# Kernel tuning notes

Measured on AMD Instinct MI355X. Metric: run time of the kernel, lower is better.

## Reference

```python
import jax, jax.numpy as jnp
import numpy as np

EPS = 1e-10


def setup_inputs() -> dict:
    key = jax.random.key(0)
    ks = jax.random.split(key, 8)
    N, C, H, W = 32, 512, 14, 14
    D, HID = 2048, 256
    s1 = 1.0 / np.sqrt(C + D)
    s2 = 1.0 / np.sqrt(HID)
    return {
        "local_feature": jax.random.normal(ks[0], (N, C, H, W), jnp.float32),
        "global_feature": jax.random.normal(ks[1], (N, D, 1, 1), jnp.float32),
        "W1": jax.random.normal(ks[2], (C + D, HID), jnp.float32) * s1,
        "b1": jnp.zeros((HID,), jnp.float32),
        "W2": jax.random.normal(ks[3], (HID, HID), jnp.float32) * s2,
        "b2": jnp.zeros((HID,), jnp.float32),
        "W3": jax.random.normal(ks[4], (HID, 1), jnp.float32) * s2,
        "b3": jnp.zeros((1,), jnp.float32),
    }


def reference(local_feature, global_feature, W1, b1, W2, b2, W3, b3):
    # Vectorized form of DMIEstimator.calculate_mi (the per-sample Python loop
    # collapsed into one batched pass with a block-diagonal negative mask).
    N, C, H, W = local_feature.shape
    hw = H * W
    nhw = N * hw
    D = global_feature.shape[1]

    lf = jnp.transpose(local_feature, (0, 2, 3, 1)).reshape(nhw, C)   # [nhw, C]
    gf = global_feature[:, :, 0, 0]                                   # [N, D]

    # combined = cat([global, local], -1); split the first Linear accordingly
    # so the [N*nhw, C+D] concat tensor is never materialized.
    h_loc = lf @ W1[D:]                        # [nhw, HID]
    h_glb = gf @ W1[:D] + b1                   # [N, HID]
    h1 = jax.nn.relu(h_glb[:, None, :] + h_loc[None, :, :])  # [N, nhw, HID]
    h2 = jax.nn.relu(h1 @ W2 + b2)                            # [N, nhw, HID]
    scores = (h2 @ W3)[..., 0] + b3[0]                        # [N, nhw]

    mx = jnp.max(scores, axis=1, keepdims=True)               # [N, 1]
    ex = jnp.exp(scores - mx)

    # negatives for sample i exclude its own hw block [hw*i, hw*(i+1))
    own = (jnp.arange(nhw)[None, :] // hw) == jnp.arange(N)[:, None]  # [N, nhw]
    neg_mean = jnp.where(own, 0.0, ex).sum(axis=1) / (nhw - hw) + EPS  # [N]

    # positive (diagonal) block of scores: scores[i, hw*i : hw*(i+1)]
    pos = scores.reshape(N, N, hw)[jnp.arange(N), jnp.arange(N)]       # [N, hw]

    mi = pos - mx - jnp.log(neg_mean)[:, None]                         # [N, hw]
    return mi.reshape(N, H, W)
```

## Files before the change

kernel.cpp:

```cpp
#include <hip/hip_runtime.h>
#include <math.h>

#define NB   32
#define CC   512
#define DD   2048
#define HWP  196
#define NHW  6272
#define HID  256

typedef _Float16 h8 __attribute__((ext_vector_type(8)));
typedef _Float16 h4 __attribute__((ext_vector_type(4)));
typedef float    f4 __attribute__((ext_vector_type(4)));
union F4H8 { f4 f; h8 h; };

__device__ __forceinline__ int fragIdx(int j, int k) {
    return ((j >> 6) << 14) + (((k >> 5) * 4 + ((j & 63) >> 4)) << 9)
         + (((((k >> 3) & 3) << 4) + (j & 15)) << 3) + (k & 7);
}

__global__ __launch_bounds__(256) void prep_kernel(const float* __restrict__ lf,
                                                   const float* __restrict__ gf,
                                                   const float* __restrict__ W1,
                                                   const float* __restrict__ W2,
                                                   float* __restrict__ hpart,
                                                   _Float16* __restrict__ W2F,
                                                   _Float16* __restrict__ W1F,
                                                   _Float16* __restrict__ lf16T) {
    int bid = blockIdx.x, tid = threadIdx.x;
    if (bid < 512) {
        int i = bid >> 4, ky = bid & 15, k = tid;
        const float* g = gf + (size_t)i * DD + ky * 128;
        const float* w = W1 + (size_t)(ky * 128) * HID + k;
        float a0 = 0.f, a1 = 0.f, a2 = 0.f, a3 = 0.f;
        #pragma unroll 8
        for (int r = 0; r < 128; r += 4) {
            a0 = fmaf(g[r + 0], w[(size_t)(r + 0) * HID], a0);
            a1 = fmaf(g[r + 1], w[(size_t)(r + 1) * HID], a1);
            a2 = fmaf(g[r + 2], w[(size_t)(r + 2) * HID], a2);
            a3 = fmaf(g[r + 3], w[(size_t)(r + 3) * HID], a3);
        }
        hpart[((size_t)i * 16 + ky) * HID + k] = (a0 + a1) + (a2 + a3);
    } else if (bid < 608) {
        int tg = (bid - 512) * 256 + tid;
        if (tg < 8192) {
            int t = tg, F = t >> 6, l = t & 63;
            int k2t = F >> 3, ks = F & 7;
            int kb = ks * 32 + (l >> 4) * 8;
            int n  = k2t * 16 + (l & 15);
            _Float16* o = W2F + (size_t)t * 8;
            #pragma unroll
            for (int j = 0; j < 8; j++) o[j] = (_Float16)W2[(size_t)(kb + j) * HID + n];
        } else {
            int t = tg - 8192, F = t >> 6, l = t & 63;
            int k2t = F >> 4, ks = F & 15;
            int kb = ks * 32 + (l >> 4) * 8;
            int n  = k2t * 16 + (l & 15);
            const float* W1c = W1 + (size_t)DD * HID;
            _Float16* o = W1F + (size_t)t * 8;
            #pragma unroll
            for (int j = 0; j < 8; j++) o[j] = (_Float16)W1c[(size_t)(kb + j) * HID + n];
        }
    } else {
        __shared__ _Float16 sT[64][HWP + 4];
        int b = bid - 608;
        int n = b >> 3, c0 = (b & 7) * 64;
        for (int task = tid; task < 64 * 49; task += 256) {
            int c = task / 49, f = task - c * 49;
            f4 v = *(const f4*)&lf[((size_t)n * CC + c0 + c) * HWP + f * 4];
            h4 o = { (_Float16)v.x, (_Float16)v.y, (_Float16)v.z, (_Float16)v.w };
            *(h4*)&sT[c][f * 4] = o;
        }
        __syncthreads();
        for (int task = tid; task < 8 * HWP; task += 256) {
            int ch = task / HWP, p = task - ch * HWP;
            h8 o;
            #pragma unroll
            for (int cc = 0; cc < 8; cc++) o[cc] = sT[ch * 8 + cc][p];
            *(h8*)&lf16T[((size_t)(n * HWP + p)) * CC + c0 + ch * 8] = o;
        }
    }
}

__global__ __launch_bounds__(256, 2) void hlocF_kernel(const _Float16* __restrict__ lf16T,
                                                       const _Float16* __restrict__ W1F,
                                                       const float* __restrict__ hpart,
                                                       const float* __restrict__ b1,
                                                       _Float16* __restrict__ g16,
                                                       _Float16* __restrict__ hF) {
    if (blockIdx.x == 196) {
        int kh = blockIdx.y;
        for (int x = threadIdx.x; x < 16 * HID; x += 256) {
            int i = kh * 16 + (x >> 8), k = x & 255;
            float s = b1[k];
            #pragma unroll
            for (int ky = 0; ky < 16; ky++) s += hpart[((size_t)i * 16 + ky) * HID + k];
            g16[(size_t)i * HID + k] = (_Float16)s;
        }
        return;
    }
    __shared__ _Float16 sLf[32][CC + 16];
    int tid = threadIdx.x;
    int w = tid >> 6, l = tid & 63, quad = l >> 4, ln = l & 15;
    int j0 = blockIdx.x * 32;
    int khalf = blockIdx.y;

    #pragma unroll
    for (int s = 0; s < 8; s++) {
        int y = s * 256 + tid;
        int row = y >> 6, col = (y & 63) * 8;
        h8 v = *(const h8*)&lf16T[(size_t)(j0 + row) * CC + col];
        *(h8*)&sLf[row][col] = v;
    }

    F4H8 Af[32];
    {
        const f4* src = (const f4*)W1F + l;
        #pragma unroll
        for (int mt = 0; mt < 2; mt++)
            #pragma unroll
            for (int ks = 0; ks < 16; ks++)
                Af[mt * 16 + ks].f = src[(size_t)((khalf * 8 + w * 2 + mt) * 16 + ks) * 64];
    }
    __syncthreads();

    f4 acc[4] = {};
    #pragma unroll
    for (int ks = 0; ks < 16; ks++) {
        h8 bF[2];
        #pragma unroll
        for (int nt = 0; nt < 2; nt++)
            bF[nt] = *(const h8*)&sLf[nt * 16 + ln][ks * 32 + quad * 8];
        #pragma unroll
        for (int mt = 0; mt < 2; mt++)
            #pragma unroll
            for (int nt = 0; nt < 2; nt++)
                acc[mt * 2 + nt] = __builtin_amdgcn_mfma_f32_16x16x32_f16(Af[mt * 16 + ks].h, bF[nt], acc[mt * 2 + nt], 0, 0, 0);
    }

    #pragma unroll
    for (int mt = 0; mt < 2; mt++)
        #pragma unroll
        for (int nt = 0; nt < 2; nt++)
            #pragma unroll
            for (int r = 0; r < 4; r++) {
                int j  = j0 + nt * 16 + ln;
                int k2 = khalf * 128 + w * 32 + mt * 16 + quad * 4 + r;
                hF[fragIdx(j, k2)] = (_Float16)acc[mt * 2 + nt][r];
            }
}

__global__ __launch_bounds__(512, 4) void score_kernel(const _Float16* __restrict__ hF,
                                                       const _Float16* __restrict__ g16,
                                                       const _Float16* __restrict__ W2F,
                                                       const float* __restrict__ b2,
                                                       const float* __restrict__ W3,
                                                       const float* __restrict__ b3,
                                                       float* __restrict__ scores) {
    __shared__ _Float16 sA[128 * HID];
    __shared__ float sRed[128][12];
    int tid = threadIdx.x, w = tid >> 6, l = tid & 63, quad = l >> 4, ln = l & 15;
    int bid = blockIdx.x;
    int i = bid & 31, jt = bid >> 5;

    F4H8 Af[16];
    {
        const f4* src = (const f4*)W2F + l;
        #pragma unroll
        for (int mt = 0; mt < 2; mt++)
            #pragma unroll
            for (int ks = 0; ks < 8; ks++)
                Af[mt * 8 + ks].f = src[(size_t)((w * 2 + mt) * 8 + ks) * 64];
    }
    const _Float16* gbase = g16 + (size_t)i * HID;
    float bias3 = b3[0];

    {
        const _Float16* hbase = hF + (size_t)(jt * 2) * 16384;
        h8 z = {};
        #pragma unroll
        for (int s = 0; s < 8; s++) {
            int y  = s * 512 + tid;
            int y2 = y & 2047;
            h8 hv = *(const h8*)&hbase[y * 8];
            h8 gq = *(const h8*)&gbase[(y2 >> 8) * 32 + ((y2 >> 4) & 3) * 8];
            *(h8*)&sA[y * 8] = __builtin_elementwise_max(hv + gq, z);
        }
    }
    __syncthreads();

    #pragma unroll 1
    for (int pass = 0; pass < 4; pass++) {
        f4 acc[4];
        #pragma unroll
        for (int mt = 0; mt < 2; mt++) {
            f4 bv = *(const f4*)&b2[w * 32 + mt * 16 + quad * 4];
            #pragma unroll
            for (int nt = 0; nt < 2; nt++) acc[mt * 2 + nt] = bv;
        }
        #pragma unroll
        for (int ks = 0; ks < 8; ks++) {
            #pragma unroll
            for (int nt = 0; nt < 2; nt++) {
                int ntg = pass * 2 + nt;
                int base = (ntg >= 4) ? 16384 + (ks * 4 + (ntg - 4)) * 512
                                      : (ks * 4 + ntg) * 512;
                h8 hz = *(const h8*)&sA[base + l * 8];
                #pragma unroll
                for (int mt = 0; mt < 2; mt++)
                    acc[mt * 2 + nt] = __builtin_amdgcn_mfma_f32_16x16x32_f16(Af[mt * 8 + ks].h, hz, acc[mt * 2 + nt], 0, 0, 0);
            }
        }
        #pragma unroll
        for (int nt = 0; nt < 2; nt++) {
            float s = 0.f;
            #pragma unroll
            for (int mt = 0; mt < 2; mt++) {
                f4 w3v = *(const f4*)&W3[w * 32 + mt * 16 + quad * 4];
                s += fmaxf(acc[mt * 2 + nt][0], 0.f) * w3v.x
                   + fmaxf(acc[mt * 2 + nt][1], 0.f) * w3v.y
                   + fmaxf(acc[mt * 2 + nt][2], 0.f) * w3v.z
                   + fmaxf(acc[mt * 2 + nt][3], 0.f) * w3v.w;
            }
            s += __shfl_xor(s, 16, 64);
            s += __shfl_xor(s, 32, 64);
            if (quad == 0) sRed[(pass * 2 + nt) * 16 + ln][w] = s;
        }
    }
    __syncthreads();
    if (tid < 128) {
        f4 a = *(const f4*)&sRed[tid][0];
        f4 b = *(const f4*)&sRed[tid][4];
        scores[(size_t)i * NHW + jt * 128 + tid] =
            a.x + a.y + a.z + a.w + b.x + b.y + b.z + b.w + bias3;
    }
}

__global__ __launch_bounds__(1024) void reduce_kernel(const float* __restrict__ scores,
                                                      float* __restrict__ out) {
    int i = blockIdx.x, tid = threadIdx.x;
    const float* row = scores + (size_t)i * NHW;
    const f4* row4 = (const f4*)row;
    __shared__ float sW[16], sW2[16], sval[2];
    float mx = -1e30f;
    for (int q = tid; q < 1568; q += 1024) {
        f4 v = row4[q];
        mx = fmaxf(mx, fmaxf(fmaxf(v.x, v.y), fmaxf(v.z, v.w)));
    }
    #pragma unroll
    for (int off = 32; off > 0; off >>= 1) mx = fmaxf(mx, __shfl_down(mx, off, 64));
    if ((tid & 63) == 0) sW[tid >> 6] = mx;
    __syncthreads();
    if (tid == 0) {
        float m = sW[0];
        for (int c = 1; c < 16; c++) m = fmaxf(m, sW[c]);
        sval[0] = m;
    }
    __syncthreads();
    mx = sval[0];
    int q0 = i * 49, q1 = q0 + 49;
    float tot = 0.f, ownv = 0.f;
    for (int q = tid; q < 1568; q += 1024) {
        f4 v = row4[q];
        float e = expf(v.x - mx) + expf(v.y - mx) + expf(v.z - mx) + expf(v.w - mx);
        tot += e;
        if (q >= q0 && q < q1) ownv += e;
    }
    #pragma unroll
    for (int off = 32; off > 0; off >>= 1) {
        tot  += __shfl_down(tot, off, 64);
        ownv += __shfl_down(ownv, off, 64);
    }
    if ((tid & 63) == 0) { sW[tid >> 6] = tot; sW2[tid >> 6] = ownv; }
    __syncthreads();
    if (tid == 0) {
        float t = 0.f, o = 0.f;
        for (int c = 0; c < 16; c++) { t += sW[c]; o += sW2[c]; }
        float neg_mean = (t - o) / (float)(NHW - HWP) + 1e-10f;
        sval[1] = mx + logf(neg_mean);
    }
    __syncthreads();
    float sub = sval[1];
    if (tid < HWP) out[(size_t)i * HWP + tid] = row[i * HWP + tid] - sub;
}

extern "C" void kernel_launch(void* const* d_in, const int* in_sizes, int n_in,
                              void* d_out, int out_size, void* d_ws, size_t ws_size,
                              hipStream_t stream) {
    const float* lf = (const float*)d_in[0];
    const float* gf = (const float*)d_in[1];
    const float* W1 = (const float*)d_in[2];
    const float* b1 = (const float*)d_in[3];
    const float* W2 = (const float*)d_in[4];
    const float* b2 = (const float*)d_in[5];
    const float* W3 = (const float*)d_in[6];
    const float* b3 = (const float*)d_in[7];
    float* out = (float*)d_out;

    char* ws = (char*)d_ws;
    _Float16* hF     = (_Float16*)ws;
    _Float16* g16    = (_Float16*)(ws + 3211264);
    _Float16* W2F    = (_Float16*)(ws + 3227648);
    _Float16* W1F    = (_Float16*)(ws + 3358720);
    _Float16* lf16T  = (_Float16*)(ws + 3620864);
    float*    scores = (float*)   (ws + 10043392);
    float*    hpart  = (float*)   (ws + 10846208);

    hipLaunchKernelGGL(prep_kernel, dim3(864), dim3(256), 0, stream,
                       lf, gf, W1, W2, hpart, W2F, W1F, lf16T);
    hipLaunchKernelGGL(hlocF_kernel, dim3(197, 2), dim3(256), 0, stream,
                       lf16T, W1F, hpart, b1, g16, hF);
    hipLaunchKernelGGL(score_kernel, dim3(1568), dim3(512), 0, stream,
                       hF, g16, W2F, b2, W3, b3, scores);
    hipLaunchKernelGGL(reduce_kernel, dim3(NB), dim3(1024), 0, stream, scores, out);
}
```

Measured before the change: 120.9 us.

## Reuse staged h_loc tile across two samples and fuse relu-add into MFMA loop

The score kernel now uses 256-thread blocks with 4 waves, each owning 64 hidden rows and holding 32 W2 fragments in registers. Each block stages its raw h_loc tile in LDS once and processes two global samples, applying the global add and ReLU on the fly right before each MFMA. This replaces the per-sample restaging and halves the per-block W2 register loads relative to the work done. hlocF output stores are also vectorized to 4-half writes. In exchange it raises register pressure (32 fragments plus 8 accumulators), redoes the add/relu per pass, and adds extra block syncs.

```diff
diff --git a/kernel.cpp b/kernel.cpp
--- a/kernel.cpp
+++ b/kernel.cpp
@@ -140,16 +140,16 @@
     #pragma unroll
     for (int mt = 0; mt < 2; mt++)
         #pragma unroll
-        for (int nt = 0; nt < 2; nt++)
-            #pragma unroll
-            for (int r = 0; r < 4; r++) {
-                int j  = j0 + nt * 16 + ln;
-                int k2 = khalf * 128 + w * 32 + mt * 16 + quad * 4 + r;
-                hF[fragIdx(j, k2)] = (_Float16)acc[mt * 2 + nt][r];
-            }
-}
-
-__global__ __launch_bounds__(512, 4) void score_kernel(const _Float16* __restrict__ hF,
+        for (int nt = 0; nt < 2; nt++) {
+            int j  = j0 + nt * 16 + ln;
+            int k2 = khalf * 128 + w * 32 + mt * 16 + quad * 4;
+            h4 o = { (_Float16)acc[mt * 2 + nt][0], (_Float16)acc[mt * 2 + nt][1],
+                     (_Float16)acc[mt * 2 + nt][2], (_Float16)acc[mt * 2 + nt][3] };
+            *(h4*)&hF[fragIdx(j, k2)] = o;
+        }
+}
+
+__global__ __launch_bounds__(256, 2) void score_kernel(const _Float16* __restrict__ hF,
                                                        const _Float16* __restrict__ g16,
                                                        const _Float16* __restrict__ W2F,
                                                        const float* __restrict__ b2,
@@ -157,81 +157,85 @@
                                                        const float* __restrict__ b3,
                                                        float* __restrict__ scores) {
     __shared__ _Float16 sA[128 * HID];
-    __shared__ float sRed[128][12];
+    __shared__ float sRed[4][132];
     int tid = threadIdx.x, w = tid >> 6, l = tid & 63, quad = l >> 4, ln = l & 15;
-    int bid = blockIdx.x;
-    int i = bid & 31, jt = bid >> 5;
-
-    F4H8 Af[16];
+    int i0 = blockIdx.x * 2, jt = blockIdx.y;
+
+    F4H8 Af[32];
     {
         const f4* src = (const f4*)W2F + l;
         #pragma unroll
-        for (int mt = 0; mt < 2; mt++)
+        for (int mt = 0; mt < 4; mt++)
             #pragma unroll
             for (int ks = 0; ks < 8; ks++)
-                Af[mt * 8 + ks].f = src[(size_t)((w * 2 + mt) * 8 + ks) * 64];
-    }
-    const _Float16* gbase = g16 + (size_t)i * HID;
+                Af[mt * 8 + ks].f = src[(size_t)((w * 4 + mt) * 8 + ks) * 64];
+    }
+    {
+        const _Float16* hbase = hF + (size_t)jt * 32768;
+        #pragma unroll
+        for (int s = 0; s < 16; s++) {
+            int y = s * 256 + tid;
+            *(h8*)&sA[y * 8] = *(const h8*)&hbase[y * 8];
+        }
+    }
     float bias3 = b3[0];
-
-    {
-        const _Float16* hbase = hF + (size_t)(jt * 2) * 16384;
-        h8 z = {};
-        #pragma unroll
-        for (int s = 0; s < 8; s++) {
-            int y  = s * 512 + tid;
-            int y2 = y & 2047;
-            h8 hv = *(const h8*)&hbase[y * 8];
-            h8 gq = *(const h8*)&gbase[(y2 >> 8) * 32 + ((y2 >> 4) & 3) * 8];
-            *(h8*)&sA[y * 8] = __builtin_elementwise_max(hv + gq, z);
-        }
-    }
+    h8 z = {};
     __syncthreads();
 
     #pragma unroll 1
-    for (int pass = 0; pass < 4; pass++) {
-        f4 acc[4];
-        #pragma unroll
-        for (int mt = 0; mt < 2; mt++) {
-            f4 bv = *(const f4*)&b2[w * 32 + mt * 16 + quad * 4];
-            #pragma unroll
-            for (int nt = 0; nt < 2; nt++) acc[mt * 2 + nt] = bv;
-        }
-        #pragma unroll
-        for (int ks = 0; ks < 8; ks++) {
+    for (int ii = 0; ii < 2; ii++) {
+        int i = i0 + ii;
+        const _Float16* gbase = g16 + (size_t)i * HID;
+        h8 gF[8];
+        #pragma unroll
+        for (int ks = 0; ks < 8; ks++)
+            gF[ks] = *(const h8*)&gbase[ks * 32 + quad * 8];
+
+        #pragma unroll 1
+        for (int pass = 0; pass < 4; pass++) {
+            f4 acc[8];
+            #pragma unroll
+            for (int mt = 0; mt < 4; mt++) {
+                f4 bv = *(const f4*)&b2[w * 64 + mt * 16 + quad * 4];
+                acc[mt * 2 + 0] = bv;
+                acc[mt * 2 + 1] = bv;
+            }
+            #pragma unroll
+            for (int ks = 0; ks < 8; ks++) {
+                #pragma unroll
+                for (int nt = 0; nt < 2; nt++) {
+                    int ntg = pass * 2 + nt;
+                    int base = (ntg >= 4) ? 16384 + (ks * 4 + (ntg - 4)) * 512
+                                          : (ks * 4 + ntg) * 512;
+                    h8 hz = *(const h8*)&sA[base + l * 8];
+                    h8 h1 = __builtin_elementwise_max(hz + gF[ks], z);
+                    #pragma unroll
+                    for (int mt = 0; mt < 4; mt++)
+                        acc[mt * 2 + nt] = __builtin_amdgcn_mfma_f32_16x16x32_f16(Af[mt * 8 + ks].h, h1, acc[mt * 2 + nt], 0, 0, 0);
+                }
+            }
             #pragma unroll
             for (int nt = 0; nt < 2; nt++) {
-                int ntg = pass * 2 + nt;
-                int base = (ntg >= 4) ? 16384 + (ks * 4 + (ntg - 4)) * 512
-                                      : (ks * 4 + ntg) * 512;
-                h8 hz = *(const h8*)&sA[base + l * 8];
+                float s = 0.f;
                 #pragma unroll
-                for (int mt = 0; mt < 2; mt++)
-                    acc[mt * 2 + nt] = __builtin_amdgcn_mfma_f32_16x16x32_f16(Af[mt * 8 + ks].h, hz, acc[mt * 2 + nt], 0, 0, 0);
+                for (int mt = 0; mt < 4; mt++) {
+                    f4 w3v = *(const f4*)&W3[w * 64 + mt * 16 + quad * 4];
+                    s += fmaxf(acc[mt * 2 + nt][0], 0.f) * w3v.x
+                       + fmaxf(acc[mt * 2 + nt][1], 0.f) * w3v.y
+                       + fmaxf(acc[mt * 2 + nt][2], 0.f) * w3v.z
+                       + fmaxf(acc[mt * 2 + nt][3], 0.f) * w3v.w;
+                }
+                s += __shfl_xor(s, 16, 64);
+                s += __shfl_xor(s, 32, 64);
+                if (quad == 0) sRed[w][(pass * 2 + nt) * 16 + ln] = s;
             }
         }
-        #pragma unroll
-        for (int nt = 0; nt < 2; nt++) {
-            float s = 0.f;
-            #pragma unroll
-            for (int mt = 0; mt < 2; mt++) {
-                f4 w3v = *(const f4*)&W3[w * 32 + mt * 16 + quad * 4];
-                s += fmaxf(acc[mt * 2 + nt][0], 0.f) * w3v.x
-                   + fmaxf(acc[mt * 2 + nt][1], 0.f) * w3v.y
-                   + fmaxf(acc[mt * 2 + nt][2], 0.f) * w3v.z
-                   + fmaxf(acc[mt * 2 + nt][3], 0.f) * w3v.w;
-            }
-            s += __shfl_xor(s, 16, 64);
-            s += __shfl_xor(s, 32, 64);
-            if (quad == 0) sRed[(pass * 2 + nt) * 16 + ln][w] = s;
-        }
-    }
-    __syncthreads();
-    if (tid < 128) {
-        f4 a = *(const f4*)&sRed[tid][0];
-        f4 b = *(const f4*)&sRed[tid][4];
-        scores[(size_t)i * NHW + jt * 128 + tid] =
-            a.x + a.y + a.z + a.w + b.x + b.y + b.z + b.w + bias3;
+        __syncthreads();
+        if (tid < 128) {
+            scores[(size_t)i * NHW + jt * 128 + tid] =
+                sRed[0][tid] + sRed[1][tid] + sRed[2][tid] + sRed[3][tid] + bias3;
+        }
+        __syncthreads();
     }
 }
 
@@ -309,7 +313,7 @@
                        lf, gf, W1, W2, hpart, W2F, W1F, lf16T);
     hipLaunchKernelGGL(hlocF_kernel, dim3(197, 2), dim3(256), 0, stream,
                        lf16T, W1F, hpart, b1, g16, hF);
-    hipLaunchKernelGGL(score_kernel, dim3(1568), dim3(512), 0, stream,
+    hipLaunchKernelGGL(score_kernel, dim3(16, 49), dim3(256), 0, stream,
                        hF, g16, W2F, b2, W3, b3, scores);
     hipLaunchKernelGGL(reduce_kernel, dim3(NB), dim3(1024), 0, stream, scores, out);
 }
```

Result: slower. 127.1 us (+5.1%).

## Retile score kernel to 64 columns × 2 samples, vectorize hF stores, online softmax reduce

Applied to the files above, without the earlier changes.

The score kernel now covers a 64-column local tile for two global samples per block. The W2 fragments loaded into registers are reused across both samples, and shared memory per block is halved, so more blocks can be resident at once. The hlocF epilogue writes four halfs in one vector store instead of four scalar stores. The reduce kernel merges its max and exp-sum passes into a single online-softmax pass. The costs are extra exps in the reduction and two more block-wide barriers per sample in the score kernel.

```diff
diff --git a/kernel.cpp b/kernel.cpp
--- a/kernel.cpp
+++ b/kernel.cpp
@@ -140,13 +140,13 @@
     #pragma unroll
     for (int mt = 0; mt < 2; mt++)
         #pragma unroll
-        for (int nt = 0; nt < 2; nt++)
-            #pragma unroll
-            for (int r = 0; r < 4; r++) {
-                int j  = j0 + nt * 16 + ln;
-                int k2 = khalf * 128 + w * 32 + mt * 16 + quad * 4 + r;
-                hF[fragIdx(j, k2)] = (_Float16)acc[mt * 2 + nt][r];
-            }
+        for (int nt = 0; nt < 2; nt++) {
+            int j  = j0 + nt * 16 + ln;
+            int k2 = khalf * 128 + w * 32 + mt * 16 + quad * 4;
+            h4 o = { (_Float16)acc[mt * 2 + nt][0], (_Float16)acc[mt * 2 + nt][1],
+                     (_Float16)acc[mt * 2 + nt][2], (_Float16)acc[mt * 2 + nt][3] };
+            *(h4*)&hF[fragIdx(j, k2)] = o;
+        }
 }
 
 __global__ __launch_bounds__(512, 4) void score_kernel(const _Float16* __restrict__ hF,
@@ -156,11 +156,10 @@
                                                        const float* __restrict__ W3,
                                                        const float* __restrict__ b3,
                                                        float* __restrict__ scores) {
-    __shared__ _Float16 sA[128 * HID];
-    __shared__ float sRed[128][12];
+    __shared__ _Float16 sA[64 * HID];
+    __shared__ float sRed[8][68];
     int tid = threadIdx.x, w = tid >> 6, l = tid & 63, quad = l >> 4, ln = l & 15;
-    int bid = blockIdx.x;
-    int i = bid & 31, jt = bid >> 5;
+    int i0 = blockIdx.x * 2, jt = blockIdx.y;
 
     F4H8 Af[16];
     {
@@ -171,67 +170,68 @@
             for (int ks = 0; ks < 8; ks++)
                 Af[mt * 8 + ks].f = src[(size_t)((w * 2 + mt) * 8 + ks) * 64];
     }
-    const _Float16* gbase = g16 + (size_t)i * HID;
+    const _Float16* hbase = hF + (size_t)jt * 16384;
     float bias3 = b3[0];
-
-    {
-        const _Float16* hbase = hF + (size_t)(jt * 2) * 16384;
-        h8 z = {};
-        #pragma unroll
-        for (int s = 0; s < 8; s++) {
-            int y  = s * 512 + tid;
-            int y2 = y & 2047;
+    h8 z = {};
+
+    #pragma unroll 1
+    for (int ii = 0; ii < 2; ii++) {
+        int i = i0 + ii;
+        const _Float16* gbase = g16 + (size_t)i * HID;
+
+        #pragma unroll
+        for (int s = 0; s < 4; s++) {
+            int y = s * 512 + tid;
             h8 hv = *(const h8*)&hbase[y * 8];
-            h8 gq = *(const h8*)&gbase[(y2 >> 8) * 32 + ((y2 >> 4) & 3) * 8];
+            h8 gq = *(const h8*)&gbase[(y >> 8) * 32 + ((y >> 4) & 3) * 8];
             *(h8*)&sA[y * 8] = __builtin_elementwise_max(hv + gq, z);
         }
-    }
-    __syncthreads();
-
-    #pragma unroll 1
-    for (int pass = 0; pass < 4; pass++) {
-        f4 acc[4];
-        #pragma unroll
-        for (int mt = 0; mt < 2; mt++) {
-            f4 bv = *(const f4*)&b2[w * 32 + mt * 16 + quad * 4];
-            #pragma unroll
-            for (int nt = 0; nt < 2; nt++) acc[mt * 2 + nt] = bv;
-        }
-        #pragma unroll
-        for (int ks = 0; ks < 8; ks++) {
+        __syncthreads();
+
+        #pragma unroll 1
+        for (int pass = 0; pass < 2; pass++) {
+            f4 acc[4];
+            #pragma unroll
+            for (int mt = 0; mt < 2; mt++) {
+                f4 bv = *(const f4*)&b2[w * 32 + mt * 16 + quad * 4];
+                acc[mt * 2 + 0] = bv;
+                acc[mt * 2 + 1] = bv;
+            }
+            #pragma unroll
+            for (int ks = 0; ks < 8; ks++) {
+                #pragma unroll
+                for (int nt = 0; nt < 2; nt++) {
+                    int ntg = pass * 2 + nt;
+                    h8 hz = *(const h8*)&sA[(ks * 4 + ntg) * 512 + l * 8];
+                    #pragma unroll
+                    for (int mt = 0; mt < 2; mt++)
+                        acc[mt * 2 + nt] = __builtin_amdgcn_mfma_f32_16x16x32_f16(Af[mt * 8 + ks].h, hz, acc[mt * 2 + nt], 0, 0, 0);
+                }
+            }
             #pragma unroll
             for (int nt = 0; nt < 2; nt++) {
-                int ntg = pass * 2 + nt;
-                int base = (ntg >= 4) ? 16384 + (ks * 4 + (ntg - 4)) * 512
-                                      : (ks * 4 + ntg) * 512;
-                h8 hz = *(const h8*)&sA[base + l * 8];
+                float s = 0.f;
                 #pragma unroll
-                for (int mt = 0; mt < 2; mt++)
-                    acc[mt * 2 + nt] = __builtin_amdgcn_mfma_f32_16x16x32_f16(Af[mt * 8 + ks].h, hz, acc[mt * 2 + nt], 0, 0, 0);
+                for (int mt = 0; mt < 2; mt++) {
+                    f4 w3v = *(const f4*)&W3[w * 32 + mt * 16 + quad * 4];
+                    s += fmaxf(acc[mt * 2 + nt][0], 0.f) * w3v.x
+                       + fmaxf(acc[mt * 2 + nt][1], 0.f) * w3v.y
+                       + fmaxf(acc[mt * 2 + nt][2], 0.f) * w3v.z
+                       + fmaxf(acc[mt * 2 + nt][3], 0.f) * w3v.w;
+                }
+                s += __shfl_xor(s, 16, 64);
+                s += __shfl_xor(s, 32, 64);
+                if (quad == 0) sRed[w][(pass * 2 + nt) * 16 + ln] = s;
             }
         }
-        #pragma unroll
-        for (int nt = 0; nt < 2; nt++) {
-            float s = 0.f;
-            #pragma unroll
-            for (int mt = 0; mt < 2; mt++) {
-                f4 w3v = *(const f4*)&W3[w * 32 + mt * 16 + quad * 4];
-                s += fmaxf(acc[mt * 2 + nt][0], 0.f) * w3v.x
-                   + fmaxf(acc[mt * 2 + nt][1], 0.f) * w3v.y
-                   + fmaxf(acc[mt * 2 + nt][2], 0.f) * w3v.z
-                   + fmaxf(acc[mt * 2 + nt][3], 0.f) * w3v.w;
-            }
-            s += __shfl_xor(s, 16, 64);
-            s += __shfl_xor(s, 32, 64);
-            if (quad == 0) sRed[(pass * 2 + nt) * 16 + ln][w] = s;
-        }
-    }
-    __syncthreads();
-    if (tid < 128) {
-        f4 a = *(const f4*)&sRed[tid][0];
-        f4 b = *(const f4*)&sRed[tid][4];
-        scores[(size_t)i * NHW + jt * 128 + tid] =
-            a.x + a.y + a.z + a.w + b.x + b.y + b.z + b.w + bias3;
+        __syncthreads();
+        if (tid < 64) {
+            float s = bias3;
+            #pragma unroll
+            for (int ww = 0; ww < 8; ww++) s += sRed[ww][tid];
+            scores[(size_t)i * NHW + jt * 64 + tid] = s;
+        }
+        __syncthreads();
     }
 }
 
@@ -240,46 +240,47 @@
     int i = blockIdx.x, tid = threadIdx.x;
     const float* row = scores + (size_t)i * NHW;
     const f4* row4 = (const f4*)row;
-    __shared__ float sW[16], sW2[16], sval[2];
-    float mx = -1e30f;
+    __shared__ float sM[16], sT[16], sO[16], sval[1];
+    int q0 = i * 49, q1 = q0 + 49;
+    float m = -1e30f, t = 0.f, o = 0.f;
     for (int q = tid; q < 1568; q += 1024) {
         f4 v = row4[q];
-        mx = fmaxf(mx, fmaxf(fmaxf(v.x, v.y), fmaxf(v.z, v.w)));
+        float vm = fmaxf(fmaxf(v.x, v.y), fmaxf(v.z, v.w));
+        float nm = fmaxf(m, vm);
+        float sc = expf(m - nm);
+        float e = expf(v.x - nm) + expf(v.y - nm) + expf(v.z - nm) + expf(v.w - nm);
+        t = t * sc + e;
+        o *= sc;
+        if (q >= q0 && q < q1) o += e;
+        m = nm;
     }
     #pragma unroll
-    for (int off = 32; off > 0; off >>= 1) mx = fmaxf(mx, __shfl_down(mx, off, 64));
-    if ((tid & 63) == 0) sW[tid >> 6] = mx;
+    for (int off = 32; off > 0; off >>= 1) {
+        float m2 = __shfl_xor(m, off, 64);
+        float t2 = __shfl_xor(t, off, 64);
+        float o2 = __shfl_xor(o, off, 64);
+        float nm = fmaxf(m, m2);
+        float sa = expf(m - nm), sb = expf(m2 - nm);
+        t = t * sa + t2 * sb;
+        o = o * sa + o2 * sb;
+        m = nm;
+    }
+    if ((tid & 63) == 0) { sM[tid >> 6] = m; sT[tid >> 6] = t; sO[tid >> 6] = o; }
     __syncthreads();
     if (tid == 0) {
-        float m = sW[0];
-        for (int c = 1; c < 16; c++) m = fmaxf(m, sW[c]);
-        sval[0] = m;
+        float M = sM[0], T = sT[0], O = sO[0];
+        for (int c = 1; c < 16; c++) {
+            float nm = fmaxf(M, sM[c]);
+            float sa = expf(M - nm), sb = expf(sM[c] - nm);
+            T = T * sa + sT[c] * sb;
+            O = O * sa + sO[c] * sb;
+            M = nm;
+        }
+        float neg_mean = (T - O) / (float)(NHW - HWP) + 1e-10f;
+        sval[0] = M + logf(neg_mean);
     }
     __syncthreads();
-    mx = sval[0];
-    int q0 = i * 49, q1 = q0 + 49;
-    float tot = 0.f, ownv = 0.f;
-    for (int q = tid; q < 1568; q += 1024) {
-        f4 v = row4[q];
-        float e = expf(v.x - mx) + expf(v.y - mx) + expf(v.z - mx) + expf(v.w - mx);
-        tot += e;
-        if (q >= q0 && q < q1) ownv += e;
-    }
-    #pragma unroll
-    for (int off = 32; off > 0; off >>= 1) {
-        tot  += __shfl_down(tot, off, 64);
-        ownv += __shfl_down(ownv, off, 64);
-    }
-    if ((tid & 63) == 0) { sW[tid >> 6] = tot; sW2[tid >> 6] = ownv; }
-    __syncthreads();
-    if (tid == 0) {
-        float t = 0.f, o = 0.f;
-        for (int c = 0; c < 16; c++) { t += sW[c]; o += sW2[c]; }
-        float neg_mean = (t - o) / (float)(NHW - HWP) + 1e-10f;
-        sval[1] = mx + logf(neg_mean);
-    }
-    __syncthreads();
-    float sub = sval[1];
+    float sub = sval[0];
     if (tid < HWP) out[(size_t)i * HWP + tid] = row[i * HWP + tid] - sub;
 }
 
@@ -309,7 +310,7 @@
                        lf, gf, W1, W2, hpart, W2F, W1F, lf16T);
     hipLaunchKernelGGL(hlocF_kernel, dim3(197, 2), dim3(256), 0, stream,
                        lf16T, W1F, hpart, b1, g16, hF);
-    hipLaunchKernelGGL(score_kernel, dim3(1568), dim3(512), 0, stream,
+    hipLaunchKernelGGL(score_kernel, dim3(16, 98), dim3(512), 0, stream,
                        hF, g16, W2F, b2, W3, b3, scores);
     hipLaunchKernelGGL(reduce_kernel, dim3(NB), dim3(1024), 0, stream, scores, out);
 }
```

After: 135.1 us. 1.12x slower.
